# Optimization experiments

Measured on AMD Instinct MI355X. Metric: run time of the kernel, lower is better.

Reference implementation:

```python
import jax, jax.numpy as jnp
import numpy as np

EPS_SIGMA = 1e-6
EPS_NORM = 1e-6


def _filters(mu_x, mu_y, sigma_x, sigma_y, W, H):
    # squash params as in forward(): tanh for means, sigmoid for sigmas
    mu_x = jnp.tanh(mu_x)
    mu_y = jnp.tanh(mu_y)
    sx = jnp.exp(1.5 - 2.0 * jax.nn.sigmoid(sigma_x))  # [N]
    sy = jnp.exp(1.5 - 2.0 * jax.nn.sigmoid(sigma_y))
    # Sigma is diagonal, so its inverse is elementwise reciprocal
    inv_x = 1.0 / (sx ** 2 + EPS_SIGMA)  # [N]
    inv_y = 1.0 / (sy ** 2 + EPS_SIGMA)
    mux = (W - 1) * ((mu_x + 1.0) / 2.0)  # [N], pixel-space mean along width
    muy = (H - 1) * ((mu_y + 1.0) / 2.0)
    xs = jnp.arange(W, dtype=jnp.float32)
    ys = jnp.arange(H, dtype=jnp.float32)
    dx = xs[None, :, None] - mux[:, None, None]  # [N,W,1]
    dy = ys[None, None, :] - muy[:, None, None]  # [N,1,H]
    quad = dx ** 2 * inv_x[:, None, None] + dy ** 2 * inv_y[:, None, None]  # [N,W,H]
    f = jnp.exp(-0.5 * quad)
    return f / (jnp.sum(f, axis=(1, 2), keepdims=True) + EPS_NORM)  # [N,W,H]


def setup_inputs() -> dict:
    key = jax.random.key(0)
    k1, k2, k3, k4, k5 = jax.random.split(key, 5)
    B, C, T, W, H, N = 8, 1024, 64, 14, 14, 3
    video = jax.random.normal(k1, (B, C, T, W, H), dtype=jnp.float32)
    mu_x = 0.5 * jax.random.normal(k2, (N,), dtype=jnp.float32)
    mu_y = 0.5 * jax.random.normal(k3, (N,), dtype=jnp.float32)
    sigma_x = 1e-4 * jax.random.normal(k4, (N,), dtype=jnp.float32)
    sigma_y = 1e-4 * jax.random.normal(k5, (N,), dtype=jnp.float32)
    return {"video": video, "mu_x": mu_x, "mu_y": mu_y,
            "sigma_x": sigma_x, "sigma_y": sigma_y}


def reference(video, mu_x, mu_y, sigma_x, sigma_y):
    B, C, T, W, H = video.shape
    f = _filters(mu_x, mu_y, sigma_x, sigma_y, W, H)  # [N,W,H]
    N = f.shape[0]
    # weighted spatial sum, then mean over time; avoids the Ni-repeated video
    o = jnp.einsum('bctwh,nwh->bcn', video, f) / T  # [B,C,N]
    return o.reshape(B, C * N)
```

## Files before the change

### kernel.cpp

```cpp
#include <hip/hip_runtime.h>
#include <math.h>

#define B_  8
#define C_  1024
#define T_  64
#define W_  14
#define H_  14
#define N_  3
#define WH  (W_ * H_)
#define WH4 (WH / 4)

__global__ void attn_pool_kernel(const float* __restrict__ video,
                                 const float* __restrict__ mu_x,
                                 const float* __restrict__ mu_y,
                                 const float* __restrict__ sigma_x,
                                 const float* __restrict__ sigma_y,
                                 float* __restrict__ out)
{
    const int wave = threadIdx.x >> 6;
    const int lane = threadIdx.x & 63;
    const int bc   = blockIdx.x * 4 + wave;

    float fv[N_][4];
#pragma unroll
    for (int n = 0; n < N_; ++n)
#pragma unroll
        for (int j = 0; j < 4; ++j) fv[n][j] = 0.0f;

    if (lane < WH4) {
#pragma unroll
        for (int n = 0; n < N_; ++n) {
            const float mux  = 6.5f * (tanhf(mu_x[n]) + 1.0f);
            const float muy  = 6.5f * (tanhf(mu_y[n]) + 1.0f);
            const float sgx  = 1.0f / (1.0f + expf(-sigma_x[n]));
            const float sgy  = 1.0f / (1.0f + expf(-sigma_y[n]));
            const float invx = 1.0f / (expf(3.0f - 4.0f * sgx) + 1e-6f);
            const float invy = 1.0f / (expf(3.0f - 4.0f * sgy) + 1e-6f);
#pragma unroll
            for (int j = 0; j < 4; ++j) {
                const int   wh = 4 * lane + j;
                const int   w  = wh / H_;
                const int   h  = wh - w * H_;
                const float dx = (float)w - mux;
                const float dy = (float)h - muy;
                fv[n][j] = expf(-0.5f * (dx * dx * invx + dy * dy * invy));
            }
        }
    }
#pragma unroll
    for (int n = 0; n < N_; ++n) {
        float s = fv[n][0] + fv[n][1] + fv[n][2] + fv[n][3];
#pragma unroll
        for (int off = 32; off > 0; off >>= 1) s += __shfl_xor(s, off);
        const float norm = 1.0f / (s + 1e-6f);
#pragma unroll
        for (int j = 0; j < 4; ++j) fv[n][j] *= norm;
    }

    const float4* v4 = (const float4*)(video + (size_t)bc * (size_t)(T_ * WH));
    float a0 = 0.0f, a1 = 0.0f, a2 = 0.0f;
    if (lane < WH4) {
#pragma unroll 8
        for (int t = 0; t < T_; ++t) {
            const float4 v = v4[t * WH4 + lane];
            a0 += v.x * fv[0][0] + v.y * fv[0][1] + v.z * fv[0][2] + v.w * fv[0][3];
            a1 += v.x * fv[1][0] + v.y * fv[1][1] + v.z * fv[1][2] + v.w * fv[1][3];
            a2 += v.x * fv[2][0] + v.y * fv[2][1] + v.z * fv[2][2] + v.w * fv[2][3];
        }
    }
#pragma unroll
    for (int off = 32; off > 0; off >>= 1) {
        a0 += __shfl_xor(a0, off);
        a1 += __shfl_xor(a1, off);
        a2 += __shfl_xor(a2, off);
    }
    if (lane == 0) {
        float* o = out + (size_t)bc * N_;
        o[0] = a0 * (1.0f / T_);
        o[1] = a1 * (1.0f / T_);
        o[2] = a2 * (1.0f / T_);
    }
}

extern "C" void kernel_launch(void* const* d_in, const int* in_sizes, int n_in,
                              void* d_out, int out_size, void* d_ws, size_t ws_size,
                              hipStream_t stream) {
    const float* video   = (const float*)d_in[0];
    const float* mu_x    = (const float*)d_in[1];
    const float* mu_y    = (const float*)d_in[2];
    const float* sigma_x = (const float*)d_in[3];
    const float* sigma_y = (const float*)d_in[4];
    float* out = (float*)d_out;

    const int waves  = B_ * C_;
    const int blocks = waves / 4;
    attn_pool_kernel<<<blocks, 256, 0, stream>>>(video, mu_x, mu_y,
                                                 sigma_x, sigma_y, out);
}
```

Measured before the change: 535.1 us.

## Flatten per-wave slab loads to use all 64 lanes with LDS filter weights

Before, each wave used only 49 of 64 lanes per timestep, so about a quarter of the lanes sat idle during the streaming loop. Now the normalized filter weights are computed once per block into shared memory, and each wave streams its contiguous slab of 3136 float4s with all 64 lanes. A rotating index finds each lane's spatial weight position. This raises memory-request efficiency for a bandwidth-bound kernel, at the cost of LDS reads per iteration and two block barriers.

```diff
diff --git a/kernel.cpp b/kernel.cpp
--- a/kernel.cpp
+++ b/kernel.cpp
@@ -1,33 +1,31 @@
 #include <hip/hip_runtime.h>
 #include <math.h>
 
-#define B_  8
-#define C_  1024
-#define T_  64
-#define W_  14
-#define H_  14
-#define N_  3
-#define WH  (W_ * H_)
-#define WH4 (WH / 4)
+#define B_    8
+#define C_    1024
+#define T_    64
+#define W_    14
+#define H_    14
+#define N_    3
+#define WH    (W_ * H_)
+#define WH4   (WH / 4)
+#define SLAB4 (T_ * WH4)
 
-__global__ void attn_pool_kernel(const float* __restrict__ video,
-                                 const float* __restrict__ mu_x,
-                                 const float* __restrict__ mu_y,
-                                 const float* __restrict__ sigma_x,
-                                 const float* __restrict__ sigma_y,
-                                 float* __restrict__ out)
+__global__ __launch_bounds__(256) void attn_pool_kernel(
+    const float* __restrict__ video,
+    const float* __restrict__ mu_x,
+    const float* __restrict__ mu_y,
+    const float* __restrict__ sigma_x,
+    const float* __restrict__ sigma_y,
+    float* __restrict__ out)
 {
-    const int wave = threadIdx.x >> 6;
-    const int lane = threadIdx.x & 63;
-    const int bc   = blockIdx.x * 4 + wave;
+    __shared__ float4 fw4[N_][WH4];
 
-    float fv[N_][4];
-#pragma unroll
-    for (int n = 0; n < N_; ++n)
-#pragma unroll
-        for (int j = 0; j < 4; ++j) fv[n][j] = 0.0f;
+    const int tid  = threadIdx.x;
+    const int wave = tid >> 6;
+    const int lane = tid & 63;
 
-    if (lane < WH4) {
+    if (tid < WH4) {
 #pragma unroll
         for (int n = 0; n < N_; ++n) {
             const float mux  = 6.5f * (tanhf(mu_x[n]) + 1.0f);
@@ -36,38 +34,60 @@
             const float sgy  = 1.0f / (1.0f + expf(-sigma_y[n]));
             const float invx = 1.0f / (expf(3.0f - 4.0f * sgx) + 1e-6f);
             const float invy = 1.0f / (expf(3.0f - 4.0f * sgy) + 1e-6f);
+            float fj[4];
 #pragma unroll
             for (int j = 0; j < 4; ++j) {
-                const int   wh = 4 * lane + j;
+                const int   wh = 4 * tid + j;
                 const int   w  = wh / H_;
                 const int   h  = wh - w * H_;
                 const float dx = (float)w - mux;
                 const float dy = (float)h - muy;
-                fv[n][j] = expf(-0.5f * (dx * dx * invx + dy * dy * invy));
+                fj[j] = expf(-0.5f * (dx * dx * invx + dy * dy * invy));
+            }
+            fw4[n][tid] = make_float4(fj[0], fj[1], fj[2], fj[3]);
+        }
+    }
+    __syncthreads();
+
+    if (wave == 0) {
+#pragma unroll
+        for (int n = 0; n < N_; ++n) {
+            float s = 0.0f;
+            float4 v;
+            if (lane < WH4) {
+                v = fw4[n][lane];
+                s = v.x + v.y + v.z + v.w;
+            }
+#pragma unroll
+            for (int off = 32; off > 0; off >>= 1) s += __shfl_xor(s, off);
+            const float inv = 1.0f / (s + 1e-6f);
+            if (lane < WH4) {
+                v.x *= inv; v.y *= inv; v.z *= inv; v.w *= inv;
+                fw4[n][lane] = v;
             }
         }
     }
-#pragma unroll
-    for (int n = 0; n < N_; ++n) {
-        float s = fv[n][0] + fv[n][1] + fv[n][2] + fv[n][3];
-#pragma unroll
-        for (int off = 32; off > 0; off >>= 1) s += __shfl_xor(s, off);
-        const float norm = 1.0f / (s + 1e-6f);
-#pragma unroll
-        for (int j = 0; j < 4; ++j) fv[n][j] *= norm;
+    __syncthreads();
+
+    const int bc = blockIdx.x * 4 + wave;
+    const float4* v4 = (const float4*)video + (size_t)bc * SLAB4;
+
+    int p = (lane < WH4) ? lane : lane - WH4;
+    float a0 = 0.0f, a1 = 0.0f, a2 = 0.0f;
+
+#pragma unroll 7
+    for (int i = 0; i < SLAB4 / 64; ++i) {
+        const float4 v  = v4[i * 64 + lane];
+        const float4 w0 = fw4[0][p];
+        const float4 w1 = fw4[1][p];
+        const float4 w2 = fw4[2][p];
+        a0 += v.x * w0.x + v.y * w0.y + v.z * w0.z + v.w * w0.w;
+        a1 += v.x * w1.x + v.y * w1.y + v.z * w1.z + v.w * w1.w;
+        a2 += v.x * w2.x + v.y * w2.y + v.z * w2.z + v.w * w2.w;
+        p += 15;
+        if (p >= WH4) p -= WH4;
     }
 
-    const float4* v4 = (const float4*)(video + (size_t)bc * (size_t)(T_ * WH));
-    float a0 = 0.0f, a1 = 0.0f, a2 = 0.0f;
-    if (lane < WH4) {
-#pragma unroll 8
-        for (int t = 0; t < T_; ++t) {
-            const float4 v = v4[t * WH4 + lane];
-            a0 += v.x * fv[0][0] + v.y * fv[0][1] + v.z * fv[0][2] + v.w * fv[0][3];
-            a1 += v.x * fv[1][0] + v.y * fv[1][1] + v.z * fv[1][2] + v.w * fv[1][3];
-            a2 += v.x * fv[2][0] + v.y * fv[2][1] + v.z * fv[2][2] + v.w * fv[2][3];
-        }
-    }
 #pragma unroll
     for (int off = 32; off > 0; off >>= 1) {
         a0 += __shfl_xor(a0, off);
```

Result: no change. 537.8 us (+0.5%).
